# Optimization experiments

Hardware: AMD Instinct MI355X
Metric: run time of the kernel (lower is better)

Reference implementation:

```python
import jax, jax.numpy as jnp
import numpy as np

B, T, D, K = 8, 4096, 512, 4096


def setup_inputs() -> dict:
    key = jax.random.key(0)
    k1, k2 = jax.random.split(key)
    x = jax.random.normal(k1, (B, T, D), dtype=jnp.float32)
    embed = jax.random.normal(k2, (K, D), dtype=jnp.float32)
    return {"x": x, "embed": embed}


def reference(x, embed):
    # F.normalize(x, p=2, dim=-1) with eps clamp like torch (eps=1e-12)
    norm = jnp.sqrt(jnp.sum(x * x, axis=-1, keepdims=True))
    xn = x / jnp.maximum(norm, 1e-12)

    flat = xn.reshape(-1, D)  # [(B*T), D]
    x_sq = jnp.sum(flat * flat, axis=1, keepdims=True)           # [(B*T), 1]
    e_sq = jnp.sum(embed * embed, axis=1)[None, :]               # [1, K]
    dist = -(x_sq - 2.0 * (flat @ embed.T) + e_sq)               # [(B*T), K]
    embed_ind = jnp.argmax(dist, axis=-1).reshape(B, T)          # [B, T]

    # decode: embedding gather then 'b n d -> b d n'
    quantize = embed[embed_ind]                                  # [B, T, D]
    quantize = jnp.transpose(quantize, (0, 2, 1))                # [B, D, T]
    return embed_ind, quantize
```

## Files before the change

kernel.cpp:

```cpp
#include <hip/hip_runtime.h>
#include <math.h>

#define BB 8
#define TT 4096
#define DDIM 512
#define KK 4096
#define NN (BB*TT)
#define EPS 0.05f
#define CMAX 16384

typedef __attribute__((ext_vector_type(8))) short bf16x8;
typedef __attribute__((ext_vector_type(4))) float f32x4;

__device__ __forceinline__ void async16(void* lds, const void* g) {
  __builtin_amdgcn_global_load_lds((const __attribute__((address_space(1))) void*)g,
                                   (__attribute__((address_space(3))) void*)lds, 16, 0, 0);
}

__device__ __forceinline__ unsigned pk_bf16(float a, float b) {
  unsigned ua = __float_as_uint(a); ua += 0x7FFFu + ((ua >> 16) & 1u);
  unsigned ub = __float_as_uint(b); ub += 0x7FFFu + ((ub >> 16) & 1u);
  return (ua >> 16) | (ub & 0xFFFF0000u);
}

__global__ __launch_bounds__(256) void prep_kernel(const float* __restrict__ x,
                                                   const float* __restrict__ embed,
                                                   short* __restrict__ xb,
                                                   short* __restrict__ eb,
                                                   float* __restrict__ inv2,
                                                   float* __restrict__ esq,
                                                   int* __restrict__ cnt) {
  if (blockIdx.x == 0 && threadIdx.x == 0) *cnt = 0;
  const float* src; short* dst; float* outv; int r; int mode;
  if (blockIdx.x < KK / 4) {
    src = embed; dst = eb; outv = esq; mode = 0;
    r = blockIdx.x * 4 + (threadIdx.x >> 6);
  } else {
    src = x; dst = xb; outv = inv2; mode = 1;
    r = (blockIdx.x - KK / 4) * 4 + (threadIdx.x >> 6);
  }
  int lane = threadIdx.x & 63;
  const float4* row4 = (const float4*)(src + (size_t)r * DDIM);
  float4 v0 = row4[lane];
  float4 v1 = row4[lane + 64];
  uint2 p0, p1;
  p0.x = pk_bf16(v0.x, v0.y); p0.y = pk_bf16(v0.z, v0.w);
  p1.x = pk_bf16(v1.x, v1.y); p1.y = pk_bf16(v1.z, v1.w);
  *(uint2*)(dst + (size_t)r * DDIM + lane * 4) = p0;
  *(uint2*)(dst + (size_t)r * DDIM + 256 + lane * 4) = p1;
  float ss = v0.x*v0.x + v0.y*v0.y + v0.z*v0.z + v0.w*v0.w
           + v1.x*v1.x + v1.y*v1.y + v1.z*v1.z + v1.w*v1.w;
  #pragma unroll
  for (int off = 32; off; off >>= 1) ss += __shfl_down(ss, off);
  if (lane == 0) outv[r] = mode ? 2.0f / fmaxf(sqrtf(ss), 1e-12f) : ss;
}

__global__ __launch_bounds__(256, 2) void vq_mfma(const short* __restrict__ xb,
                                                  const short* __restrict__ eb,
                                                  const float* __restrict__ esq,
                                                  const float* __restrict__ inv2,
                                                  float4* __restrict__ top2) {
  __shared__ short As[128 * 64];
  __shared__ short Bs[256 * 64];
  __shared__ float rS1[2][128];
  __shared__ float rS2[2][128];
  __shared__ int   rI1[2][128];

  const int tid = threadIdx.x;
  const int lane = tid & 63;
  const int w = tid >> 6;
  const int wr = w >> 1, wc = w & 1;
  const int q = lane >> 4, c16 = lane & 15;

  const int mb = blockIdx.x & 255;
  const int kq = blockIdx.x >> 8;
  const int n0 = mb * 128;
  const int kbase = kq * 1024;

  const int srow = lane >> 3;
  const int scol = ((lane & 7) ^ srow) * 8;
  const short* gA = xb + (size_t)(n0 + w * 32 + srow) * DDIM + scol;

  float s1[16], s2v[16];
  int   i1[16];
  #pragma unroll
  for (int s = 0; s < 16; ++s) { s1[s] = -3e38f; s2v[s] = -3e38f; i1[s] = 0; }

  f32x4 inv4[4];
  #pragma unroll
  for (int ti = 0; ti < 4; ++ti)
    inv4[ti] = *(const f32x4*)&inv2[n0 + wr * 64 + ti * 16 + q * 4];

  for (int c = 0; c < 4; ++c) {
    const int k0c = kbase + c * 256;
    const short* gB = eb + (size_t)(k0c + w * 64 + srow) * DDIM + scol;
    f32x4 acc[4][8];
    #pragma unroll
    for (int ti = 0; ti < 4; ++ti)
      #pragma unroll
      for (int tj = 0; tj < 8; ++tj) acc[ti][tj] = (f32x4){0.f, 0.f, 0.f, 0.f};

    for (int d0 = 0; d0 < DDIM; d0 += 64) {
      #pragma unroll
      for (int i = 0; i < 4; ++i)
        async16(As + (w * 32 + i * 8) * 64, gA + (size_t)i * 8 * DDIM + d0);
      #pragma unroll
      for (int i = 0; i < 8; ++i)
        async16(Bs + (w * 64 + i * 8) * 64, gB + (size_t)i * 8 * DDIM + d0);
      __syncthreads();
      #pragma unroll
      for (int ks = 0; ks < 2; ++ks) {
        const int ko = (((ks << 2) | q) ^ (lane & 7)) << 3;
        bf16x8 af[4];
        #pragma unroll
        for (int ti = 0; ti < 4; ++ti)
          af[ti] = *(const bf16x8*)&As[(wr * 64 + ti * 16 + c16) * 64 + ko];
        #pragma unroll
        for (int h = 0; h < 2; ++h) {
          bf16x8 bf[4];
          #pragma unroll
          for (int j = 0; j < 4; ++j)
            bf[j] = *(const bf16x8*)&Bs[(wc * 128 + (h * 4 + j) * 16 + c16) * 64 + ko];
          #pragma unroll
          for (int ti = 0; ti < 4; ++ti)
            #pragma unroll
            for (int j = 0; j < 4; ++j)
              acc[ti][h * 4 + j] = __builtin_amdgcn_mfma_f32_16x16x32_bf16(
                  af[ti], bf[j], acc[ti][h * 4 + j], 0, 0, 0);
        }
      }
      __syncthreads();
    }
    #pragma unroll
    for (int tj = 0; tj < 8; ++tj) {
      const int col = k0c + wc * 128 + tj * 16 + c16;
      const float nes = -esq[col];
      #pragma unroll
      for (int ti = 0; ti < 4; ++ti)
        #pragma unroll
        for (int r = 0; r < 4; ++r) {
          int slot = ti * 4 + r;
          float sc = fmaf(acc[ti][tj][r], inv4[ti][r], nes);
          float mn = fminf(sc, s1[slot]);
          s2v[slot] = fmaxf(s2v[slot], mn);
          if (sc > s1[slot]) { s1[slot] = sc; i1[slot] = col; }
        }
    }
  }

  #pragma unroll
  for (int slot = 0; slot < 16; ++slot) {
    float a1 = s1[slot], a2 = s2v[slot]; int ai = i1[slot];
    #pragma unroll
    for (int off = 1; off < 16; off <<= 1) {
      float b1 = __shfl_xor(a1, off);
      float b2 = __shfl_xor(a2, off);
      int   bi = __shfl_xor(ai, off);
      float mn = fminf(a1, b1);
      a2 = fmaxf(fmaxf(a2, b2), mn);
      if (b1 > a1 || (b1 == a1 && bi < ai)) { a1 = b1; ai = bi; }
    }
    if (c16 == 0) {
      int row = wr * 64 + (slot >> 2) * 16 + q * 4 + (slot & 3);
      rS1[wc][row] = a1; rS2[wc][row] = a2; rI1[wc][row] = ai;
    }
  }
  __syncthreads();
  if (tid < 128) {
    float a1 = rS1[0][tid], a2 = rS2[0][tid]; int ai = rI1[0][tid];
    float b1 = rS1[1][tid], b2 = rS2[1][tid]; int bi = rI1[1][tid];
    float mn = fminf(a1, b1);
    a2 = fmaxf(fmaxf(a2, b2), mn);
    if (b1 > a1 || (b1 == a1 && bi < ai)) { a1 = b1; ai = bi; }
    top2[(size_t)kq * NN + n0 + tid] = make_float4(a1, __int_as_float(ai), a2, 0.f);
  }
}

__global__ __launch_bounds__(256) void finalize_kernel(const float4* __restrict__ top2,
                                                       float* __restrict__ out_ind,
                                                       int* __restrict__ flags,
                                                       int* __restrict__ list,
                                                       int* __restrict__ cnt) {
  int row = blockIdx.x * 256 + threadIdx.x;
  float a1 = -3e38f, a2 = -3e38f; int ai = 0;
  #pragma unroll
  for (int kq = 0; kq < 4; ++kq) {
    float4 t = top2[(size_t)kq * NN + row];
    float b1 = t.x, b2 = t.z; int bi = __float_as_int(t.y);
    float mn = fminf(a1, b1);
    a2 = fmaxf(fmaxf(a2, b2), mn);
    if (b1 > a1 || (b1 == a1 && bi < ai)) { a1 = b1; ai = bi; }
  }
  out_ind[row] = (float)ai;
  int f = 0;
  if (a1 - a2 < EPS) {
    int p = atomicAdd(cnt, 1);
    if (p < CMAX) { list[p] = row; f = p + 1; }
  }
  flags[row] = f;
}

__global__ __launch_bounds__(256) void cleanup_kernel(const float* __restrict__ x,
                                                      const float* __restrict__ embed,
                                                      const float* __restrict__ esq,
                                                      const float* __restrict__ inv2,
                                                      const int* __restrict__ list,
                                                      const int* __restrict__ cnt,
                                                      float2* __restrict__ exact) {
  __shared__ float xr[16][DDIM];
  __shared__ float xiv[16];
  __shared__ int   rid[16];
  __shared__ float red_s[4][16];
  __shared__ int   red_i[4][16];
  const int kc = blockIdx.x >> 5;
  const int slot = blockIdx.x & 31;
  const int tid = threadIdx.x;
  const int lane = tid & 63, w = tid >> 6;
  int n = *cnt; if (n > CMAX) n = CMAX;
  const int code = kc * 256 + tid;
  const float4* erow = (const float4*)&embed[(size_t)code * DDIM];
  const float nes = -esq[code];

  for (int tile = slot; tile * 16 < n; tile += 32) {
    __syncthreads();
    if (tid < 16) {
      int pos = tile * 16 + tid;
      int row = (pos < n) ? list[pos] : list[0];
      rid[tid] = row;
      xiv[tid] = inv2[row];
    }
    __syncthreads();
    #pragma unroll
    for (int i = 0; i < 8; ++i) {
      int idx = tid + i * 256;
      int rl = idx >> 7, d4 = idx & 127;
      ((float4*)xr[rl])[d4] = *(const float4*)&x[(size_t)rid[rl] * DDIM + d4 * 4];
    }
    __syncthreads();
    float acc[16];
    #pragma unroll
    for (int r = 0; r < 16; ++r) acc[r] = 0.f;
    for (int d4 = 0; d4 < 128; ++d4) {
      float4 e4 = erow[d4];
      #pragma unroll
      for (int r = 0; r < 16; ++r) {
        float4 x4 = ((const float4*)xr[r])[d4];
        acc[r] += e4.x * x4.x + e4.y * x4.y + e4.z * x4.z + e4.w * x4.w;
      }
    }
    #pragma unroll
    for (int r = 0; r < 16; ++r) {
      float bs = fmaf(acc[r], xiv[r], nes);
      int bi = code;
      #pragma unroll
      for (int off = 1; off < 64; off <<= 1) {
        float b1 = __shfl_xor(bs, off);
        int   b2 = __shfl_xor(bi, off);
        if (b1 > bs || (b1 == bs && b2 < bi)) { bs = b1; bi = b2; }
      }
      if (lane == 0) { red_s[w][r] = bs; red_i[w][r] = bi; }
    }
    __syncthreads();
    if (tid < 16) {
      float bs = red_s[0][tid]; int bi = red_i[0][tid];
      #pragma unroll
      for (int ww = 1; ww < 4; ++ww) {
        float b1 = red_s[ww][tid]; int b2 = red_i[ww][tid];
        if (b1 > bs || (b1 == bs && b2 < bi)) { bs = b1; bi = b2; }
      }
      int pos = tile * 16 + tid;
      if (pos < n) exact[(size_t)pos * 16 + kc] = make_float2(bs, (float)bi);
    }
  }
}

__global__ __launch_bounds__(256) void gather_kernel(const float* __restrict__ embed,
                                                     const int* __restrict__ flags,
                                                     const float2* __restrict__ exact,
                                                     float* __restrict__ out_ind,
                                                     float* __restrict__ out_q) {
  __shared__ int lidx[64];
  __shared__ float trans[64 * 65];
  const int n0 = blockIdx.x * 64;
  const int tid = threadIdx.x;
  if (tid < 64) {
    const int row = n0 + tid;
    const int f = flags[row];
    int idx;
    if (f) {
      float bsv = -3e38f; int bi = 0;
      const float2* e16 = &exact[(size_t)(f - 1) * 16];
      #pragma unroll
      for (int k = 0; k < 16; ++k) {
        float2 t = e16[k];
        int ci = (int)t.y;
        if (t.x > bsv || (t.x == bsv && ci < bi)) { bsv = t.x; bi = ci; }
      }
      idx = bi;
      out_ind[row] = (float)idx;
    } else {
      idx = (int)out_ind[row];
    }
    lidx[tid] = idx;
  }
  __syncthreads();
  const int bb = n0 >> 12;
  const int t0 = n0 & (TT - 1);
  const int w = tid >> 6, lane = tid & 63;
  for (int d0 = 0; d0 < DDIM; d0 += 64) {
    if (d0) __syncthreads();
    #pragma unroll
    for (int qq = 0; qq < 16; ++qq) {
      int tt2 = w * 16 + qq;
      int e = lidx[tt2];
      trans[lane * 65 + tt2] = embed[(size_t)e * DDIM + d0 + lane];
    }
    __syncthreads();
    #pragma unroll
    for (int qq = 0; qq < 4; ++qq) {
      int dl = (tid >> 4) * 4 + qq;
      int t4 = (tid & 15) * 4;
      float4 o;
      o.x = trans[dl * 65 + t4 + 0];
      o.y = trans[dl * 65 + t4 + 1];
      o.z = trans[dl * 65 + t4 + 2];
      o.w = trans[dl * 65 + t4 + 3];
      *(float4*)&out_q[((size_t)bb * DDIM + d0 + dl) * TT + t0 + t4] = o;
    }
  }
}

extern "C" void kernel_launch(void* const* d_in, const int* in_sizes, int n_in,
                              void* d_out, int out_size, void* d_ws, size_t ws_size,
                              hipStream_t stream) {
  const float* x     = (const float*)d_in[0];
  const float* embed = (const float*)d_in[1];
  char* ws = (char*)d_ws;
  short* xb      = (short*)(ws);
  short* eb      = (short*)(ws + 33554432);
  float* esq     = (float*)(ws + 37748736);
  float* inv2    = (float*)(ws + 37765120);
  float4* top2   = (float4*)(ws + 37896192);
  int* list      = (int*)(ws + 39993344);
  int* flags     = (int*)(ws + 40058880);
  float2* exact  = (float2*)(ws + 40189952);
  int* cnt       = (int*)(ws + 42287104);

  float* out_ind = (float*)d_out;
  float* out_q   = out_ind + NN;

  prep_kernel<<<KK / 4 + NN / 4, 256, 0, stream>>>(x, embed, xb, eb, inv2, esq, cnt);
  vq_mfma<<<1024, 256, 0, stream>>>(xb, eb, esq, inv2, top2);
  finalize_kernel<<<NN / 256, 256, 0, stream>>>(top2, out_ind, flags, list, cnt);
  cleanup_kernel<<<512, 256, 0, stream>>>(x, embed, esq, inv2, list, cnt, exact);
  gather_kernel<<<NN / 64, 256, 0, stream>>>(embed, flags, exact, out_ind, out_q);
}
```

Measured before the change: 348.7 us.

## Shrink codebook tile to 128 columns, raise occupancy, issue next tile's loads early

The main MFMA kernel now works on 128x128 output tiles instead of 128x256. This halves the B shared-memory buffer and the accumulator registers, so launch bounds can request 4 blocks per SIMD instead of 2. Global-to-LDS loads for the next (chunk, d) step are issued right after the compute barrier, so they overlap the epilogue and the loop overhead. The candidate-rescoring margin EPS is also tightened, which sends fewer rows to the exact fp32 recheck but slightly raises the risk of a wrong argmax. The A tile is reloaded twice as often per codebook column, which adds global and LDS traffic.

```diff
diff --git a/kernel.cpp b/kernel.cpp
--- a/kernel.cpp
+++ b/kernel.cpp
@@ -6,7 +6,7 @@
 #define DDIM 512
 #define KK 4096
 #define NN (BB*TT)
-#define EPS 0.05f
+#define EPS 0.035f
 #define CMAX 16384
 
 typedef __attribute__((ext_vector_type(8))) short bf16x8;
@@ -55,13 +55,13 @@
   if (lane == 0) outv[r] = mode ? 2.0f / fmaxf(sqrtf(ss), 1e-12f) : ss;
 }
 
-__global__ __launch_bounds__(256, 2) void vq_mfma(const short* __restrict__ xb,
+__global__ __launch_bounds__(256, 4) void vq_mfma(const short* __restrict__ xb,
                                                   const short* __restrict__ eb,
                                                   const float* __restrict__ esq,
                                                   const float* __restrict__ inv2,
                                                   float4* __restrict__ top2) {
   __shared__ short As[128 * 64];
-  __shared__ short Bs[256 * 64];
+  __shared__ short Bs[128 * 64];
   __shared__ float rS1[2][128];
   __shared__ float rS2[2][128];
   __shared__ int   rI1[2][128];
@@ -77,9 +77,10 @@
   const int n0 = mb * 128;
   const int kbase = kq * 1024;
 
-  const int srow = lane >> 3;
-  const int scol = ((lane & 7) ^ srow) * 8;
-  const short* gA = xb + (size_t)(n0 + w * 32 + srow) * DDIM + scol;
+  const int srow = w * 32 + (lane >> 3);
+  const int scol = ((lane & 7) ^ (lane >> 3)) * 8;
+  const short* gA = xb + (size_t)(n0 + srow) * DDIM + scol;
+  const short* gBb = eb + (size_t)(kbase + srow) * DDIM + scol;
 
   float s1[16], s2v[16];
   int   i1[16];
@@ -91,49 +92,50 @@
   for (int ti = 0; ti < 4; ++ti)
     inv4[ti] = *(const f32x4*)&inv2[n0 + wr * 64 + ti * 16 + q * 4];
 
-  for (int c = 0; c < 4; ++c) {
-    const int k0c = kbase + c * 256;
-    const short* gB = eb + (size_t)(k0c + w * 64 + srow) * DDIM + scol;
-    f32x4 acc[4][8];
+  auto issue = [&](int t) {
+    const int c = t >> 3, d0 = (t & 7) * 64;
+    #pragma unroll
+    for (int i = 0; i < 4; ++i) {
+      async16(As + (w * 32 + i * 8) * 64, gA + (size_t)i * 8 * DDIM + d0);
+      async16(Bs + (w * 32 + i * 8) * 64,
+              gBb + (size_t)(c * 128 + i * 8) * DDIM + d0);
+    }
+  };
+
+  issue(0);
+  for (int c = 0; c < 8; ++c) {
+    const int k0c = kbase + c * 128;
+    f32x4 acc[4][4];
     #pragma unroll
     for (int ti = 0; ti < 4; ++ti)
       #pragma unroll
-      for (int tj = 0; tj < 8; ++tj) acc[ti][tj] = (f32x4){0.f, 0.f, 0.f, 0.f};
-
-    for (int d0 = 0; d0 < DDIM; d0 += 64) {
-      #pragma unroll
-      for (int i = 0; i < 4; ++i)
-        async16(As + (w * 32 + i * 8) * 64, gA + (size_t)i * 8 * DDIM + d0);
-      #pragma unroll
-      for (int i = 0; i < 8; ++i)
-        async16(Bs + (w * 64 + i * 8) * 64, gB + (size_t)i * 8 * DDIM + d0);
+      for (int tj = 0; tj < 4; ++tj) acc[ti][tj] = (f32x4){0.f, 0.f, 0.f, 0.f};
+
+    for (int d = 0; d < 8; ++d) {
       __syncthreads();
       #pragma unroll
       for (int ks = 0; ks < 2; ++ks) {
         const int ko = (((ks << 2) | q) ^ (lane & 7)) << 3;
-        bf16x8 af[4];
+        bf16x8 af[4], bf[4];
         #pragma unroll
         for (int ti = 0; ti < 4; ++ti)
           af[ti] = *(const bf16x8*)&As[(wr * 64 + ti * 16 + c16) * 64 + ko];
         #pragma unroll
-        for (int h = 0; h < 2; ++h) {
-          bf16x8 bf[4];
+        for (int tj = 0; tj < 4; ++tj)
+          bf[tj] = *(const bf16x8*)&Bs[(wc * 64 + tj * 16 + c16) * 64 + ko];
+        #pragma unroll
+        for (int ti = 0; ti < 4; ++ti)
           #pragma unroll
-          for (int j = 0; j < 4; ++j)
-            bf[j] = *(const bf16x8*)&Bs[(wc * 128 + (h * 4 + j) * 16 + c16) * 64 + ko];
-          #pragma unroll
-          for (int ti = 0; ti < 4; ++ti)
-            #pragma unroll
-            for (int j = 0; j < 4; ++j)
-              acc[ti][h * 4 + j] = __builtin_amdgcn_mfma_f32_16x16x32_bf16(
-                  af[ti], bf[j], acc[ti][h * 4 + j], 0, 0, 0);
-        }
+          for (int tj = 0; tj < 4; ++tj)
+            acc[ti][tj] = __builtin_amdgcn_mfma_f32_16x16x32_bf16(af[ti], bf[tj], acc[ti][tj], 0, 0, 0);
       }
       __syncthreads();
-    }
-    #pragma unroll
-    for (int tj = 0; tj < 8; ++tj) {
-      const int col = k0c + wc * 128 + tj * 16 + c16;
+      int t = c * 8 + d + 1;
+      if (t < 64) issue(t);
+    }
+    #pragma unroll
+    for (int tj = 0; tj < 4; ++tj) {
+      const int col = k0c + wc * 64 + tj * 16 + c16;
       const float nes = -esq[col];
       #pragma unroll
       for (int ti = 0; ti < 4; ++ti)
```

Result: slower. 560.1 us (+60.6%).
